# Kernel tuning notes

Measured on AMD Instinct MI355X. Metric: run time of the kernel, lower is better.

The kernel has to match this reference:

```python
import jax, jax.numpy as jnp
import numpy as np


def _conv1x1(x, w):
    # x [N,I,D,H,W], w [O,I]
    return jnp.einsum('nidhw,oi->nodhw', x, w)


def _conv3x3(x, w):
    return jax.lax.conv_general_dilated(
        x, w, window_strides=(1, 1, 1), padding=[(1, 1)] * 3,
        dimension_numbers=('NCDHW', 'OIDHW', 'NCDHW'))


def _interp_axis(x, out_len, axis):
    # linear interpolation along one axis, align_corners=True
    in_len = x.shape[axis]
    scale = (in_len - 1) / (out_len - 1)
    pos = jnp.arange(out_len, dtype=x.dtype) * scale
    lo = jnp.clip(jnp.floor(pos).astype(jnp.int32), 0, in_len - 1)
    hi = jnp.minimum(lo + 1, in_len - 1)
    frac = pos - lo.astype(x.dtype)
    shp = [1] * x.ndim
    shp[axis] = out_len
    frac = frac.reshape(shp)
    return jnp.take(x, lo, axis=axis) * (1 - frac) + jnp.take(x, hi, axis=axis) * frac


def _upsample_trilinear_ac(x, size):
    for ax, s in zip((2, 3, 4), size):
        x = _interp_axis(x, s, ax)
    return x


def _grid_sample_3d(inp, grid):
    # inp [N,C,D,H,W]; grid [N,Do,Ho,Wo,3] with channels (x=w, y=h, z=d) in [-1,1]
    # matches torch grid_sample defaults: trilinear, align_corners=False, zeros padding
    N, C, D, H, W = inp.shape
    ix = ((grid[..., 0] + 1) * W - 1) * 0.5
    iy = ((grid[..., 1] + 1) * H - 1) * 0.5
    iz = ((grid[..., 2] + 1) * D - 1) * 0.5
    x0 = jnp.floor(ix).astype(jnp.int32)
    y0 = jnp.floor(iy).astype(jnp.int32)
    z0 = jnp.floor(iz).astype(jnp.int32)
    fx = ix - x0.astype(inp.dtype)
    fy = iy - y0.astype(inp.dtype)
    fz = iz - z0.astype(inp.dtype)
    flat = inp.reshape(N, C, D * H * W)
    out = jnp.zeros((N, C) + grid.shape[1:4], dtype=inp.dtype)
    for dz, wz in ((0, 1 - fz), (1, fz)):
        for dy, wy in ((0, 1 - fy), (1, fy)):
            for dx, wx in ((0, 1 - fx), (1, fx)):
                zc = z0 + dz
                yc = y0 + dy
                xc = x0 + dx
                valid = (zc >= 0) & (zc < D) & (yc >= 0) & (yc < H) & (xc >= 0) & (xc < W)
                idx = (jnp.clip(zc, 0, D - 1) * H + jnp.clip(yc, 0, H - 1)) * W + jnp.clip(xc, 0, W - 1)
                vals = jax.vmap(lambda f, i: f[:, i])(flat, idx)  # [N,C,Do,Ho,Wo]
                w = (wz * wy * wx) * valid.astype(inp.dtype)
                out = out + vals * w[:, None]
    return out


def _point_reinforce(x, w_atten, w_conv):
    # SE-style: global avg pool -> 1x1 conv -> sigmoid -> residual scale -> 1x1 conv
    pooled = jnp.mean(x, axis=(2, 3, 4), keepdims=True)
    atten = jax.nn.sigmoid(_conv1x1(pooled, w_atten))
    x = x + x * atten
    return _conv1x1(x, w_conv)


def _forward(x, y, w_down_h, w_down_l, w_flow, w_att_atten, w_att_conv):
    D, H, W = x.shape[2:]
    low = _conv1x1(x, w_down_l)
    low = _point_reinforce(low, w_att_atten, w_att_conv)
    hf = _conv1x1(y, w_down_h)
    hf = _upsample_trilinear_ac(hf, (D, H, W))
    flow = _conv3x3(jnp.concatenate([hf, low], axis=1), w_flow)  # [N,3,D,H,W]
    # coordinate grid, channel order (w, h, d) as in the original flow_warp
    gw = jnp.broadcast_to(jnp.arange(W, dtype=x.dtype)[None, None, :], (D, H, W))
    gh = jnp.broadcast_to(jnp.arange(H, dtype=x.dtype)[None, :, None], (D, H, W))
    gd = jnp.broadcast_to(jnp.arange(D, dtype=x.dtype)[:, None, None], (D, H, W))
    grid = jnp.stack([gw, gh, gd], axis=0)[None]  # [1,3,D,H,W]
    norm = jnp.array([W, H, D], dtype=x.dtype)
    # NOTE: faithful to original -- divides by size only (grid ends up in [0,1), not [-1,1])
    vgrid = jnp.transpose(grid + flow, (0, 2, 3, 4, 1)) / norm  # [N,D,H,W,3]
    return _grid_sample_3d(y, vgrid)


def setup_inputs() -> dict:
    key = jax.random.key(0)
    ks = jax.random.split(key, 7)
    inplane_l, inplane_h, outplane = 64, 128, 64
    x = jax.random.normal(ks[0], (2, inplane_l, 16, 64, 64), dtype=jnp.float32)
    y = jax.random.normal(ks[1], (2, inplane_h, 8, 32, 32), dtype=jnp.float32)
    s = 0.05
    w_down_h = jax.random.normal(ks[2], (outplane, inplane_h), dtype=jnp.float32) * s
    w_down_l = jax.random.normal(ks[3], (outplane, inplane_l), dtype=jnp.float32) * s
    w_flow = jax.random.normal(ks[4], (3, 2 * outplane, 3, 3, 3), dtype=jnp.float32) * s
    w_att_atten = jax.random.normal(ks[5], (inplane_l, inplane_l), dtype=jnp.float32) * s
    w_att_conv = jax.random.normal(ks[6], (inplane_l, inplane_l), dtype=jnp.float32) * s
    return {'x': x, 'y': y, 'w_down_h': w_down_h, 'w_down_l': w_down_l,
            'w_flow': w_flow, 'w_att_atten': w_att_atten, 'w_att_conv': w_att_conv}


def reference(x, y, w_down_h, w_down_l, w_flow, w_att_atten, w_att_conv):
    return _forward(x, y, w_down_h, w_down_l, w_flow, w_att_atten, w_att_conv)
```

## Files before the change

kernel.cpp:

```cpp
#include <hip/hip_runtime.h>
#include <math.h>


#define MEANX_OFF  0
#define WEFF_OFF   128
#define HF_OFF     16384
#define HFUP_OFF   1064960
#define VG_OFF     9453568
#define ZPAGE_OFF  9846784

__global__ __launch_bounds__(256) void kearly(const float* __restrict__ x,
                                              const float* __restrict__ y,
                                              const float* __restrict__ wdh,
                                              float* __restrict__ meanx,
                                              float* __restrict__ hf,
                                              float* __restrict__ zpage) {
    const int blk = blockIdx.x;
    if (blk < 128) {
        if (blk == 0 && threadIdx.x < 64) zpage[threadIdx.x] = 0.f;
        int ch = blk;
        const float4* base = (const float4*)(x + (size_t)ch * 65536);
        float s = 0.f;
        for (int j = threadIdx.x; j < 16384; j += 256) {
            float4 v = base[j];
            s += v.x + v.y + v.z + v.w;
        }
        __shared__ float red[256];
        red[threadIdx.x] = s;
        __syncthreads();
        for (int off = 128; off > 0; off >>= 1) {
            if (threadIdx.x < off) red[threadIdx.x] += red[threadIdx.x + off];
            __syncthreads();
        }
        if (threadIdx.x == 0) meanx[ch] = red[0] * (1.0f / 65536.0f);
    } else {
        const int b = blk - 128;
        const int n = b >> 7;
        const int r = b & 127;
        const int os = r & 3;
        const int tile = r >> 2;
        const int p = tile * 256 + threadIdx.x;
        const float* yb = y + (size_t)n * 128 * 8192 + p;

        float acc[16];
#pragma unroll
        for (int o = 0; o < 16; ++o) acc[o] = 0.f;

        for (int i = 0; i < 128; i += 4) {
            const float yi0 = yb[(size_t)(i + 0) * 8192];
            const float yi1 = yb[(size_t)(i + 1) * 8192];
            const float yi2 = yb[(size_t)(i + 2) * 8192];
            const float yi3 = yb[(size_t)(i + 3) * 8192];
#pragma unroll
            for (int o = 0; o < 16; ++o) {
                float a = acc[o];
                a = fmaf(wdh[(os * 16 + o) * 128 + i + 0], yi0, a);
                a = fmaf(wdh[(os * 16 + o) * 128 + i + 1], yi1, a);
                a = fmaf(wdh[(os * 16 + o) * 128 + i + 2], yi2, a);
                a = fmaf(wdh[(os * 16 + o) * 128 + i + 3], yi3, a);
                acc[o] = a;
            }
        }
        float* ob = hf + (size_t)(n * 64 + os * 16) * 8192 + p;
#pragma unroll
        for (int o = 0; o < 16; ++o)
            ob[(size_t)o * 8192] = acc[o];
    }
}

__global__ __launch_bounds__(256) void kprep(const float* __restrict__ wdl,
                                             const float* __restrict__ watt,
                                             const float* __restrict__ wconv,
                                             const float* __restrict__ wflow,
                                             const float* __restrict__ meanx,
                                             float* __restrict__ weff) {
    const int n = blockIdx.x;
    const int tid = threadIdx.x;
    __shared__ float s_wdl[4096];
    __shared__ float s_wcT[4096];
    __shared__ float s_flow[5184];
    __shared__ float pooled[64], sc[64];
    for (int k = tid; k < 4096; k += 256) {
        s_wdl[k] = wdl[k];
        int o = k >> 6, j = k & 63;
        s_wcT[j * 64 + o] = wconv[k];
    }
    for (int k = tid; k < 5184; k += 256) {
        int o = k / 1728, r = k - o * 1728;
        s_flow[k] = wflow[o * 3456 + 1728 + r];
    }
    __syncthreads();
    if (tid < 64) {
        float p = 0.f;
        for (int i = 0; i < 64; ++i) p += s_wdl[tid * 64 + i] * meanx[n * 64 + i];
        pooled[tid] = p;
    }
    __syncthreads();
    if (tid < 64) {
        float a = 0.f;
        for (int i = 0; i < 64; ++i) a += watt[tid * 64 + i] * pooled[i];
        sc[tid] = 1.f + 1.f / (1.f + expf(-a));
    }
    __syncthreads();
    float wc[16];
#pragma unroll
    for (int k = 0; k < 16; ++k) {
        const int idx = tid + 256 * k;
        const int o = idx & 63, i = idx >> 6;
        float acc = 0.f;
#pragma unroll 8
        for (int j = 0; j < 64; ++j)
            acc += s_wcT[j * 64 + o] * (sc[j] * s_wdl[j * 64 + i]);
        wc[k] = acc;
    }
    __syncthreads();
#pragma unroll
    for (int k = 0; k < 16; ++k) {
        const int idx = tid + 256 * k;
        const int o = idx & 63, i = idx >> 6;
        s_wdl[i * 64 + o] = wc[k];
    }
    __syncthreads();
    for (int e = tid; e < 5184; e += 256) {
        const int i = e / 81, r = e - i * 81;
        const int o = r / 27, tap = r - o * 27;
        float acc = 0.f;
#pragma unroll 8
        for (int c = 0; c < 64; ++c)
            acc += s_flow[o * 1728 + c * 27 + tap] * s_wdl[i * 64 + c];
        weff[n * 5184 + e] = acc;
    }
}

__global__ __launch_bounds__(256) void kmid(const float* __restrict__ hf,
                                            float* __restrict__ hfup) {
    int id2 = blockIdx.x * 256 + threadIdx.x;
    int wp = id2 & 31, h = (id2 >> 5) & 63, d = (id2 >> 11) & 15;
    int c = (id2 >> 15) & 63, n = id2 >> 21;
    const float SD = 7.0f / 15.0f, SH = 31.0f / 63.0f;
    float pd = (float)d * SD, ph = (float)h * SH;
    int z0 = (int)pd; if (z0 > 7) z0 = 7;
    int z1 = min(z0 + 1, 7); float fz = pd - (float)z0;
    int y0 = (int)ph; if (y0 > 31) y0 = 31;
    int y1 = min(y0 + 1, 31); float fy = ph - (float)y0;

    const int w0i = 2 * wp, w1i = 2 * wp + 1;
    float pw0 = (float)w0i * SH, pw1 = (float)w1i * SH;
    int xa = (int)pw0; if (xa > 31) xa = 31;
    float fx0 = pw0 - (float)xa;
    int xb2 = (int)pw1; if (xb2 > 31) xb2 = 31;
    float fx1 = pw1 - (float)xb2;

    const float* b = hf + (size_t)(n * 64 + c) * 8192;
    const int r00 = (z0 * 32 + y0) * 32, r01 = (z0 * 32 + y1) * 32;
    const int r10 = (z1 * 32 + y0) * 32, r11 = (z1 * 32 + y1) * 32;
    const float wzy00 = (1.f - fz) * (1.f - fy), wzy01 = (1.f - fz) * fy;
    const float wzy10 = fz * (1.f - fy), wzy11 = fz * fy;

    float colv[3];
#pragma unroll
    for (int j = 0; j < 3; ++j) {
        int xc = min(xa + j, 31);
        colv[j] = wzy00 * b[r00 + xc] + wzy01 * b[r01 + xc] +
                  wzy10 * b[r10 + xc] + wzy11 * b[r11 + xc];
    }
    float o0 = colv[0] + (colv[1] - colv[0]) * fx0;
    int i1 = xb2 - xa;
    float lo = (i1 == 0) ? colv[0] : colv[1];
    float hi = (i1 == 0) ? colv[1] : colv[2];
    float o1 = lo + (hi - lo) * fx1;

    *(float2*)(hfup + ((size_t)id2 * 2)) = make_float2(o0, o1);
}

__global__ __launch_bounds__(256) void kflowp(const float* __restrict__ ws,
                                              const float* __restrict__ x,
                                              const float* __restrict__ wflow,
                                              const float* __restrict__ weff,
                                              float* __restrict__ part) {
    const int tid = threadIdx.x;
    const int b = blockIdx.x;
    const int split = b & 15;
    const int tile = b >> 4;
    const int n = tile >> 6;
    const int t = tile & 63;
    const int td = t >> 4, th = (t >> 2) & 3, tw = t & 3;
    const int d0 = td * 4, h0 = th * 16, w0 = tw * 16;
    const int xo = tid & 3, ty = (tid >> 2) & 15, tz = tid >> 6;
    const int wv = tid >> 6;

    __shared__ float lds[3][2048];

    const float* gb = (split < 8)
        ? ws + HFUP_OFF + (size_t)(n * 64 + split * 8) * 65536
        : x + (size_t)(n * 64 + (split - 8) * 8) * 65536;
    const float* zp = ws + ZPAGE_OFF;

    const float* addrk[8];
    int strk[8];
#pragma unroll
    for (int k = 0; k < 8; ++k) {
        const int e = tid + 256 * k;
        const int r = e / 18;
        const int lx = e - r * 18;
        const int z = r / 18;
        const int ly = r - z * 18;
        const int gz = d0 - 1 + z, gy = h0 - 1 + ly, gx = w0 - 1 + lx;
        const bool ok = (e < 1944) && ((unsigned)gz < 16u) && ((unsigned)gy < 64u) &&
                        ((unsigned)gx < 64u);
        addrk[k] = ok ? (gb + (gz * 4096 + gy * 64 + gx)) : zp;
        strk[k] = ok ? 65536 : 0;
    }

#define STAGE(BUFI, CI)                                                               \
    {                                                                                 \
        _Pragma("unroll")                                                             \
        for (int k = 0; k < 8; ++k) {                                                 \
            __builtin_amdgcn_global_load_lds(                                         \
                (const __attribute__((address_space(1))) unsigned int*)               \
                    (addrk[k] + (size_t)(CI) * strk[k]),                              \
                (__attribute__((address_space(3))) unsigned int*)                     \
                    (&lds[BUFI][wv * 64 + 256 * k]),                                  \
                4, 0, 0);                                                             \
        }                                                                             \
    }

    float acc[3][4];
#pragma unroll
    for (int o = 0; o < 3; ++o)
#pragma unroll
        for (int j = 0; j < 4; ++j) acc[o][j] = 0.f;

    STAGE(0, 0);

    for (int ci = 0; ci < 8; ++ci) {
        const int cur = ci % 3;
        if (ci < 7) {
            STAGE((ci + 1) % 3, ci + 1);
            asm volatile("s_waitcnt vmcnt(8)" ::: "memory");
        } else {
            asm volatile("s_waitcnt vmcnt(0)" ::: "memory");
        }
        __builtin_amdgcn_s_barrier();
        __builtin_amdgcn_sched_barrier(0);

        const int cidx = __builtin_amdgcn_readfirstlane(
            (split < 8) ? (split * 8 + ci) : ((split - 8) * 8 + ci));
        const float* wbase;
        int wos;
        if (split < 8) { wbase = wflow + (size_t)cidx * 27; wos = 3456; }
        else           { wbase = weff + (size_t)n * 5184 + (size_t)cidx * 81; wos = 27; }
        const float* buf = lds[cur];
#pragma unroll
        for (int dz = 0; dz < 3; ++dz) {
#pragma unroll
            for (int dy = 0; dy < 3; ++dy) {
                const float* rp = &buf[((tz + dz) * 18 + ty + dy) * 18 + 4 * xo];
                const float2 a0 = *(const float2*)(rp);
                const float2 a1 = *(const float2*)(rp + 2);
                const float2 a2 = *(const float2*)(rp + 4);
                const float v[6] = {a0.x, a0.y, a1.x, a1.y, a2.x, a2.y};
                float wq[3][3];
#pragma unroll
                for (int o = 0; o < 3; ++o)
#pragma unroll
                    for (int dx = 0; dx < 3; ++dx)
                        wq[o][dx] = wbase[o * wos + (dz * 3 + dy) * 3 + dx];
#pragma unroll
                for (int o = 0; o < 3; ++o)
#pragma unroll
                    for (int j = 0; j < 4; ++j)
#pragma unroll
                        for (int dx = 0; dx < 3; ++dx)
                            acc[o][j] = fmaf(wq[o][dx], v[j + dx], acc[o][j]);
            }
        }
    }
#undef STAGE

    const int oz = d0 + tz, oy = h0 + ty, ox = w0 + 4 * xo;
    const size_t base = ((size_t)(split * 2 + n)) * 3 * 65536;
    const int p = oz * 4096 + oy * 64 + ox;
#pragma unroll
    for (int o = 0; o < 3; ++o)
        *(float4*)(part + base + (size_t)o * 65536 + p) =
            make_float4(acc[o][0], acc[o][1], acc[o][2], acc[o][3]);
}

__global__ __launch_bounds__(256) void kpost(const float* __restrict__ part,
                                             const float* __restrict__ y,
                                             float* __restrict__ vg,
                                             float* __restrict__ yt) {
    const int blk = blockIdx.x;
    if (blk < 128) {
        int gid = blk * 256 + threadIdx.x;
        int n = gid >> 14, p4 = (gid & 16383) * 4;
        float4 s0 = make_float4(0.f, 0.f, 0.f, 0.f);
        float4 s1 = s0, s2 = s0;
        for (int s = 0; s < 16; ++s) {
            const float* bp = part + ((size_t)(s * 2 + n)) * 3 * 65536 + p4;
            float4 a = *(const float4*)(bp);
            float4 b4 = *(const float4*)(bp + 65536);
            float4 c4 = *(const float4*)(bp + 131072);
            s0.x += a.x; s0.y += a.y; s0.z += a.z; s0.w += a.w;
            s1.x += b4.x; s1.y += b4.y; s1.z += b4.z; s1.w += b4.w;
            s2.x += c4.x; s2.y += c4.y; s2.z += c4.z; s2.w += c4.w;
        }
        int w = p4 & 63, h = (p4 >> 6) & 63, d = p4 >> 12;
        size_t vb = (size_t)n * 3 * 65536;
        *(float4*)(vg + vb + p4) = make_float4(
            ((float)(w + 0) + s0.x) * (1.0f / 64.0f), ((float)(w + 1) + s0.y) * (1.0f / 64.0f),
            ((float)(w + 2) + s0.z) * (1.0f / 64.0f), ((float)(w + 3) + s0.w) * (1.0f / 64.0f));
        *(float4*)(vg + vb + 65536 + p4) = make_float4(
            ((float)h + s1.x) * (1.0f / 64.0f), ((float)h + s1.y) * (1.0f / 64.0f),
            ((float)h + s1.z) * (1.0f / 64.0f), ((float)h + s1.w) * (1.0f / 64.0f));
        *(float4*)(vg + vb + 131072 + p4) = make_float4(
            ((float)d + s2.x) * (1.0f / 16.0f), ((float)d + s2.y) * (1.0f / 16.0f),
            ((float)d + s2.z) * (1.0f / 16.0f), ((float)d + s2.w) * (1.0f / 16.0f));
    } else {
        int b = blk - 128;
        int n = b >> 8;
        int rem = b & 255;
        int ct = rem >> 7, st = rem & 127;
        int c0 = ct * 64, s0 = st * 64;
        __shared__ float t[64][65];
        int tx = threadIdx.x & 63, ty = threadIdx.x >> 6;
#pragma unroll
        for (int k = 0; k < 16; ++k)
            t[ty + 4 * k][tx] = y[((size_t)(n * 128 + c0 + ty + 4 * k)) * 8192 + s0 + tx];
        __syncthreads();
#pragma unroll
        for (int k = 0; k < 16; ++k)
            yt[((size_t)(n * 8192 + s0 + ty + 4 * k)) * 128 + c0 + tx] = t[tx][ty + 4 * k];
    }
}

__global__ __launch_bounds__(256) void ksample(const float* __restrict__ yt,
                                               const float* __restrict__ vg,
                                               float* __restrict__ out) {
    const int b = blockIdx.x;
    const int n = b >> 10;
    const int p0 = (b & 1023) << 6;
    const int tid = threadIdx.x;
    const int lane = tid & 63;
    const int wv = tid >> 6;

    __shared__ float lds[128 * 65];

    const float* ytn = yt + (size_t)n * 8192 * 128;
    const size_t vb = (size_t)n * 3 * 65536;

    for (int q = 0; q < 16; ++q) {
        const int pt = wv * 16 + q;
        const int p = p0 + pt;
        float gx = vg[vb + p], gy = vg[vb + 65536 + p], gz = vg[vb + 131072 + p];
        float ix = ((gx + 1.f) * 32.f - 1.f) * 0.5f;
        float iy = ((gy + 1.f) * 32.f - 1.f) * 0.5f;
        float iz = ((gz + 1.f) * 8.f - 1.f) * 0.5f;
        int x0 = (int)floorf(ix), y0 = (int)floorf(iy), z0 = (int)floorf(iz);
        float fx = ix - (float)x0, fy = iy - (float)y0, fz = iz - (float)z0;
        float wx[2] = {1.f - fx, fx}, wy[2] = {1.f - fy, fy}, wz[2] = {1.f - fz, fz};
        int idx8[8];
        float w8[8];
        float wsum = 0.f;
#pragma unroll
        for (int k = 0; k < 8; ++k) {
            int dz = k >> 2, dy = (k >> 1) & 1, dx = k & 1;
            int zc = z0 + dz, yc = y0 + dy, xc = x0 + dx;
            bool valid = ((unsigned)zc < 8u) && ((unsigned)yc < 32u) && ((unsigned)xc < 32u);
            int zcl = min(max(zc, 0), 7), ycl = min(max(yc, 0), 31), xcl = min(max(xc, 0), 31);
            idx8[k] = (zcl * 32 + ycl) * 32 + xcl;
            float wgt = wz[dz] * wy[dy] * wx[dx];
            w8[k] = valid ? wgt : 0.f;
            wsum += w8[k];
        }
        float ax = 0.f, ay = 0.f;
        if (wsum != 0.f) {
#pragma unroll
            for (int k = 0; k < 8; ++k) {
                const float2 v = *(const float2*)(ytn + (size_t)idx8[k] * 128 + 2 * lane);
                ax = fmaf(w8[k], v.x, ax);
                ay = fmaf(w8[k], v.y, ay);
            }
        }
        lds[(2 * lane) * 65 + pt] = ax;
        lds[(2 * lane + 1) * 65 + pt] = ay;
    }
    __syncthreads();
    const int pw = tid & 63, cw = tid >> 6;
    float* ob = out + (size_t)n * 128 * 65536 + p0 + pw;
#pragma unroll
    for (int k = 0; k < 32; ++k) {
        int c = k * 4 + cw;
        ob[(size_t)c * 65536] = lds[c * 65 + pw];
    }
}

extern "C" void kernel_launch(void* const* d_in, const int* in_sizes, int n_in,
                              void* d_out, int out_size, void* d_ws, size_t ws_size,
                              hipStream_t stream) {
    const float* x     = (const float*)d_in[0];
    const float* y     = (const float*)d_in[1];
    const float* wdh   = (const float*)d_in[2];
    const float* wdl   = (const float*)d_in[3];
    const float* wflow = (const float*)d_in[4];
    const float* watt  = (const float*)d_in[5];
    const float* wconv = (const float*)d_in[6];
    float* out = (float*)d_out;

    float* ws     = (float*)d_ws;
    float* meanx  = ws + MEANX_OFF;
    float* weff   = ws + WEFF_OFF;
    float* hf     = ws + HF_OFF;
    float* hfup   = ws + HFUP_OFF;
    float* vg     = ws + VG_OFF;
    float* zpage  = ws + ZPAGE_OFF;

    float* part = out;
    float* yt = hfup;

    kearly<<<384, 256, 0, stream>>>(x, y, wdh, meanx, hf, zpage);
    kprep<<<2, 256, 0, stream>>>(wdl, watt, wconv, wflow, meanx, weff);
    kmid<<<16384, 256, 0, stream>>>(hf, hfup);
    kflowp<<<2048, 256, 0, stream>>>(ws, x, wflow, weff, part);
    kpost<<<640, 256, 0, stream>>>(part, y, vg, yt);
    ksample<<<2048, 256, 0, stream>>>(yt, vg, out);
}
```

Measured before the change: 178.4 us.

## Move x-branch flow conv partials into upsample kernel to overlap independent work

The flow conv's x-branch channel splits, which depend only on x and the effective weights rather than the upsampled features, now run as an extra 1024 blocks inside the upsample kernel. This lets that compute-heavy work overlap with the memory-bound trilinear upsample instead of waiting behind it. The remaining flow kernel handles only the hfup half with half the blocks and uses 32-bit offsets from the workspace base. The added cost is a larger mixed kernel whose conv blocks use LDS, which may lower occupancy for the upsample blocks.

```diff
diff --git a/kernel.cpp b/kernel.cpp
--- a/kernel.cpp
+++ b/kernel.cpp
@@ -132,56 +132,162 @@
     }
 }
 
-__global__ __launch_bounds__(256) void kmid(const float* __restrict__ hf,
-                                            float* __restrict__ hfup) {
-    int id2 = blockIdx.x * 256 + threadIdx.x;
-    int wp = id2 & 31, h = (id2 >> 5) & 63, d = (id2 >> 11) & 15;
-    int c = (id2 >> 15) & 63, n = id2 >> 21;
-    const float SD = 7.0f / 15.0f, SH = 31.0f / 63.0f;
-    float pd = (float)d * SD, ph = (float)h * SH;
-    int z0 = (int)pd; if (z0 > 7) z0 = 7;
-    int z1 = min(z0 + 1, 7); float fz = pd - (float)z0;
-    int y0 = (int)ph; if (y0 > 31) y0 = 31;
-    int y1 = min(y0 + 1, 31); float fy = ph - (float)y0;
-
-    const int w0i = 2 * wp, w1i = 2 * wp + 1;
-    float pw0 = (float)w0i * SH, pw1 = (float)w1i * SH;
-    int xa = (int)pw0; if (xa > 31) xa = 31;
-    float fx0 = pw0 - (float)xa;
-    int xb2 = (int)pw1; if (xb2 > 31) xb2 = 31;
-    float fx1 = pw1 - (float)xb2;
-
-    const float* b = hf + (size_t)(n * 64 + c) * 8192;
-    const int r00 = (z0 * 32 + y0) * 32, r01 = (z0 * 32 + y1) * 32;
-    const int r10 = (z1 * 32 + y0) * 32, r11 = (z1 * 32 + y1) * 32;
-    const float wzy00 = (1.f - fz) * (1.f - fy), wzy01 = (1.f - fz) * fy;
-    const float wzy10 = fz * (1.f - fy), wzy11 = fz * fy;
-
-    float colv[3];
-#pragma unroll
-    for (int j = 0; j < 3; ++j) {
-        int xc = min(xa + j, 31);
-        colv[j] = wzy00 * b[r00 + xc] + wzy01 * b[r01 + xc] +
-                  wzy10 * b[r10 + xc] + wzy11 * b[r11 + xc];
-    }
-    float o0 = colv[0] + (colv[1] - colv[0]) * fx0;
-    int i1 = xb2 - xa;
-    float lo = (i1 == 0) ? colv[0] : colv[1];
-    float hi = (i1 == 0) ? colv[1] : colv[2];
-    float o1 = lo + (hi - lo) * fx1;
-
-    *(float2*)(hfup + ((size_t)id2 * 2)) = make_float2(o0, o1);
+__global__ __launch_bounds__(256) void kmid(const float* __restrict__ x,
+                                            const float* __restrict__ ws,
+                                            const float* __restrict__ weff,
+                                            const float* __restrict__ hf,
+                                            float* __restrict__ hfup,
+                                            float* __restrict__ part) {
+    const int blk = blockIdx.x;
+    if (blk < 1024) {
+        const int tid = threadIdx.x;
+        const int sp = blk & 7;
+        const int tile = blk >> 3;
+        const int n = tile >> 6;
+        const int t = tile & 63;
+        const int td = t >> 4, th = (t >> 2) & 3, tw = t & 3;
+        const int d0 = td * 4, h0 = th * 16, w0 = tw * 16;
+        const int xo = tid & 3, ty = (tid >> 2) & 15, tz = tid >> 6;
+        const int wv = tid >> 6;
+
+        __shared__ float lds[3][2048];
+
+        const float* gb = x + (size_t)(n * 64 + sp * 8) * 65536;
+        const float* zp = ws + ZPAGE_OFF;
+
+        const float* addrk[8];
+        int vmask = 0;
+#pragma unroll
+        for (int k = 0; k < 8; ++k) {
+            const int e = tid + 256 * k;
+            const int r = e / 18;
+            const int lx = e - r * 18;
+            const int z = r / 18;
+            const int ly = r - z * 18;
+            const int gz = d0 - 1 + z, gy = h0 - 1 + ly, gx = w0 - 1 + lx;
+            const bool ok = (e < 1944) && ((unsigned)gz < 16u) && ((unsigned)gy < 64u) &&
+                            ((unsigned)gx < 64u);
+            addrk[k] = ok ? (gb + (gz * 4096 + gy * 64 + gx)) : zp;
+            vmask |= (ok ? 1 : 0) << k;
+        }
+
+#define STAGEL(BUFI)                                                                  \
+    {                                                                                 \
+        _Pragma("unroll")                                                             \
+        for (int k = 0; k < 8; ++k) {                                                 \
+            __builtin_amdgcn_global_load_lds(                                         \
+                (const __attribute__((address_space(1))) unsigned int*)(addrk[k]),    \
+                (__attribute__((address_space(3))) unsigned int*)                     \
+                    (&lds[BUFI][wv * 64 + 256 * k]),                                  \
+                4, 0, 0);                                                             \
+            addrk[k] += ((vmask >> k) & 1) ? 65536 : 0;                               \
+        }                                                                             \
+    }
+
+        float acc[3][4];
+#pragma unroll
+        for (int o = 0; o < 3; ++o)
+#pragma unroll
+            for (int j = 0; j < 4; ++j) acc[o][j] = 0.f;
+
+        STAGEL(0);
+
+        for (int ci = 0; ci < 8; ++ci) {
+            const int cur = ci % 3;
+            if (ci < 7) {
+                STAGEL((ci + 1) % 3);
+                asm volatile("s_waitcnt vmcnt(8)" ::: "memory");
+            } else {
+                asm volatile("s_waitcnt vmcnt(0)" ::: "memory");
+            }
+            __builtin_amdgcn_s_barrier();
+            __builtin_amdgcn_sched_barrier(0);
+
+            const int cidx = __builtin_amdgcn_readfirstlane(sp * 8 + ci);
+            const float* wbase = weff + (size_t)n * 5184 + (size_t)cidx * 81;
+            const float* buf = lds[cur];
+#pragma unroll
+            for (int dz = 0; dz < 3; ++dz) {
+#pragma unroll
+                for (int dy = 0; dy < 3; ++dy) {
+                    const float* rp = &buf[((tz + dz) * 18 + ty + dy) * 18 + 4 * xo];
+                    const float2 a0 = *(const float2*)(rp);
+                    const float2 a1 = *(const float2*)(rp + 2);
+                    const float2 a2 = *(const float2*)(rp + 4);
+                    const float v[6] = {a0.x, a0.y, a1.x, a1.y, a2.x, a2.y};
+                    float wq[3][3];
+#pragma unroll
+                    for (int o = 0; o < 3; ++o)
+#pragma unroll
+                        for (int dx = 0; dx < 3; ++dx)
+                            wq[o][dx] = wbase[o * 27 + (dz * 3 + dy) * 3 + dx];
+#pragma unroll
+                    for (int o = 0; o < 3; ++o)
+#pragma unroll
+                        for (int j = 0; j < 4; ++j)
+#pragma unroll
+                            for (int dx = 0; dx < 3; ++dx)
+                                acc[o][j] = fmaf(wq[o][dx], v[j + dx], acc[o][j]);
+                }
+            }
+        }
+#undef STAGEL
+
+        const int oz = d0 + tz, oy = h0 + ty, ox = w0 + 4 * xo;
+        const size_t base = ((size_t)((sp + 8) * 2 + n)) * 3 * 65536;
+        const int p = oz * 4096 + oy * 64 + ox;
+#pragma unroll
+        for (int o = 0; o < 3; ++o)
+            *(float4*)(part + base + (size_t)o * 65536 + p) =
+                make_float4(acc[o][0], acc[o][1], acc[o][2], acc[o][3]);
+    } else {
+        int id2 = (blk - 1024) * 256 + threadIdx.x;
+        int wp = id2 & 31, h = (id2 >> 5) & 63, d = (id2 >> 11) & 15;
+        int c = (id2 >> 15) & 63, n = id2 >> 21;
+        const float SD = 7.0f / 15.0f, SH = 31.0f / 63.0f;
+        float pd = (float)d * SD, ph = (float)h * SH;
+        int z0 = (int)pd; if (z0 > 7) z0 = 7;
+        int z1 = min(z0 + 1, 7); float fz = pd - (float)z0;
+        int y0 = (int)ph; if (y0 > 31) y0 = 31;
+        int y1 = min(y0 + 1, 31); float fy = ph - (float)y0;
+
+        const int w0i = 2 * wp, w1i = 2 * wp + 1;
+        float pw0 = (float)w0i * SH, pw1 = (float)w1i * SH;
+        int xa = (int)pw0; if (xa > 31) xa = 31;
+        float fx0 = pw0 - (float)xa;
+        int xb2 = (int)pw1; if (xb2 > 31) xb2 = 31;
+        float fx1 = pw1 - (float)xb2;
+
+        const float* b = hf + (size_t)(n * 64 + c) * 8192;
+        const int r00 = (z0 * 32 + y0) * 32, r01 = (z0 * 32 + y1) * 32;
+        const int r10 = (z1 * 32 + y0) * 32, r11 = (z1 * 32 + y1) * 32;
+        const float wzy00 = (1.f - fz) * (1.f - fy), wzy01 = (1.f - fz) * fy;
+        const float wzy10 = fz * (1.f - fy), wzy11 = fz * fy;
+
+        float colv[3];
+#pragma unroll
+        for (int j = 0; j < 3; ++j) {
+            int xc = min(xa + j, 31);
+            colv[j] = wzy00 * b[r00 + xc] + wzy01 * b[r01 + xc] +
+                      wzy10 * b[r10 + xc] + wzy11 * b[r11 + xc];
+        }
+        float o0 = colv[0] + (colv[1] - colv[0]) * fx0;
+        int i1 = xb2 - xa;
+        float lo = (i1 == 0) ? colv[0] : colv[1];
+        float hi = (i1 == 0) ? colv[1] : colv[2];
+        float o1 = lo + (hi - lo) * fx1;
+
+        *(float2*)(hfup + ((size_t)id2 * 2)) = make_float2(o0, o1);
+    }
 }
 
 __global__ __launch_bounds__(256) void kflowp(const float* __restrict__ ws,
-                                              const float* __restrict__ x,
                                               const float* __restrict__ wflow,
-                                              const float* __restrict__ weff,
                                               float* __restrict__ part) {
     const int tid = threadIdx.x;
     const int b = blockIdx.x;
-    const int split = b & 15;
-    const int tile = b >> 4;
+    const int split = b & 7;
+    const int tile = b >> 3;
     const int n = tile >> 6;
     const int t = tile & 63;
     const int td = t >> 4, th = (t >> 2) & 3, tw = t & 3;
@@ -191,13 +297,9 @@
 
     __shared__ float lds[3][2048];
 
-    const float* gb = (split < 8)
-        ? ws + HFUP_OFF + (size_t)(n * 64 + split * 8) * 65536
-        : x + (size_t)(n * 64 + (split - 8) * 8) * 65536;
-    const float* zp = ws + ZPAGE_OFF;
-
-    const float* addrk[8];
-    int strk[8];
+    const int srcb = HFUP_OFF + (n * 64 + split * 8) * 65536;
+
+    int woff[8];
 #pragma unroll
     for (int k = 0; k < 8; ++k) {
         const int e = tid + 256 * k;
@@ -208,17 +310,16 @@
         const int gz = d0 - 1 + z, gy = h0 - 1 + ly, gx = w0 - 1 + lx;
         const bool ok = (e < 1944) && ((unsigned)gz < 16u) && ((unsigned)gy < 64u) &&
                         ((unsigned)gx < 64u);
-        addrk[k] = ok ? (gb + (gz * 4096 + gy * 64 + gx)) : zp;
-        strk[k] = ok ? 65536 : 0;
+        woff[k] = ok ? (srcb + gz * 4096 + gy * 64 + gx) : ZPAGE_OFF;
     }
 
 #define STAGE(BUFI, CI)                                                               \
     {                                                                                 \
         _Pragma("unroll")                                                             \
         for (int k = 0; k < 8; ++k) {                                                 \
+            const int off = woff[k] + ((woff[k] < ZPAGE_OFF) ? (CI) * 65536 : 0);     \
             __builtin_amdgcn_global_load_lds(                                         \
-                (const __attribute__((address_space(1))) unsigned int*)               \
-                    (addrk[k] + (size_t)(CI) * strk[k]),                              \
+                (const __attribute__((address_space(1))) unsigned int*)(ws + off),    \
                 (__attribute__((address_space(3))) unsigned int*)                     \
                     (&lds[BUFI][wv * 64 + 256 * k]),                                  \
                 4, 0, 0);                                                             \
@@ -244,12 +345,8 @@
         __builtin_amdgcn_s_barrier();
         __builtin_amdgcn_sched_barrier(0);
 
-        const int cidx = __builtin_amdgcn_readfirstlane(
-            (split < 8) ? (split * 8 + ci) : ((split - 8) * 8 + ci));
-        const float* wbase;
-        int wos;
-        if (split < 8) { wbase = wflow + (size_t)cidx * 27; wos = 3456; }
-        else           { wbase = weff + (size_t)n * 5184 + (size_t)cidx * 81; wos = 27; }
+        const int cgs = __builtin_amdgcn_readfirstlane(split * 8 + ci);
+        const float* wb = wflow + (size_t)cgs * 27;
         const float* buf = lds[cur];
 #pragma unroll
         for (int dz = 0; dz < 3; ++dz) {
@@ -265,7 +362,7 @@
                 for (int o = 0; o < 3; ++o)
 #pragma unroll
                     for (int dx = 0; dx < 3; ++dx)
-                        wq[o][dx] = wbase[o * wos + (dz * 3 + dy) * 3 + dx];
+                        wq[o][dx] = wb[o * 3456 + (dz * 3 + dy) * 3 + dx];
 #pragma unroll
                 for (int o = 0; o < 3; ++o)
 #pragma unroll
@@ -421,8 +518,8 @@
 
     kearly<<<384, 256, 0, stream>>>(x, y, wdh, meanx, hf, zpage);
     kprep<<<2, 256, 0, stream>>>(wdl, watt, wconv, wflow, meanx, weff);
-    kmid<<<16384, 256, 0, stream>>>(hf, hfup);
-    kflowp<<<2048, 256, 0, stream>>>(ws, x, wflow, weff, part);
+    kmid<<<17408, 256, 0, stream>>>(x, ws, weff, hf, hfup, part);
+    kflowp<<<1024, 256, 0, stream>>>(ws, wflow, part);
     kpost<<<640, 256, 0, stream>>>(part, y, vg, yt);
     ksample<<<2048, 256, 0, stream>>>(yt, vg, out);
 }
```

After: 172.6 us. 1.03x faster.
